# Kernel optimization log

Hardware: AMD Instinct MI355X
Metric: run time of the kernel (lower is better)

The kernel has to match this reference:

```python
import jax, jax.numpy as jnp
import numpy as np

B, S, T, H, NH, G, E, I, R, L = 256, 256, 16, 1024, 8, 3, 8, 4096, 256, 3
GTEMP, RTEMP, TOPK_G, NEG = 1.0, 1.0, 2, -1e9

_W = {
    'ts_in_w': (3*H, H), 'ts_out_w': (H, H),
    'st_in_w': (3*H, H), 'st_out_w': (H, H),
    'ca_in_w': (3*H, H), 'ca_out_w': (H, H),
    'opq_w': (H, H), 'fuse_w': (H, 3*H), 'gate_w': (H, 3*H),
    'bs_w': (R, H), 'bt_w': (R, H), 'bo_w': (H, R),
    'cond_w': (H, 2*H), 'gr_w': (G, H), 'er_w': (G, E, H),
    'e_w1': (G, E, I, H), 'e_w2': (G, E, H, I), 'cls_w': (L, H),
}
_B = {
    'ts_in_b': (3*H,), 'ts_out_b': (H,), 'st_in_b': (3*H,), 'st_out_b': (H,),
    'ca_in_b': (3*H,), 'ca_out_b': (H,), 'fuse_b': (H,), 'gate_b': (H,),
    'bs_b': (R,), 'bt_b': (R,), 'bo_b': (H,), 'cond_b': (H,),
    'gr_b': (G,), 'er_b': (G, E), 'e_b1': (G, E, I), 'e_b2': (G, E, H),
    'cls_b': (L,), 'ln_b': (3*H,),
}


def setup_inputs() -> dict:
    key = jax.random.key(0)
    out = {}
    out['h_sent'] = jax.random.normal(jax.random.fold_in(key, 1), (B, S, H), dtype=jnp.float32)
    out['h_term'] = jax.random.normal(jax.random.fold_in(key, 2), (B, T, H), dtype=jnp.float32)
    for i, (name, shp) in enumerate(_W.items()):
        out[name] = 0.02 * jax.random.normal(jax.random.fold_in(key, 100 + i), shp, dtype=jnp.float32)
    for name, shp in _B.items():
        out[name] = jnp.zeros(shp, dtype=jnp.float32)
    out['ln_g'] = jnp.ones((3*H,), dtype=jnp.float32)
    return out


def _mha(q, k, v, w_in, b_in, w_out, b_out):
    # torch nn.MultiheadAttention (batch_first, eval mode / no dropout)
    wq, wk, wv = jnp.split(w_in, 3, axis=0)
    bq, bk, bv = jnp.split(b_in, 3, axis=0)
    Q, K, V = q @ wq.T + bq, k @ wk.T + bk, v @ wv.T + bv
    b, lq, _ = Q.shape
    lk = K.shape[1]
    d = H // NH
    Q = Q.reshape(b, lq, NH, d).transpose(0, 2, 1, 3)
    K = K.reshape(b, lk, NH, d).transpose(0, 2, 1, 3)
    V = V.reshape(b, lk, NH, d).transpose(0, 2, 1, 3)
    att = jax.nn.softmax(jnp.einsum('bhqd,bhkd->bhqk', Q, K) * (1.0 / d ** 0.5), axis=-1)
    o = jnp.einsum('bhqk,bhkd->bhqd', att, V).transpose(0, 2, 1, 3).reshape(b, lq, H)
    return o @ w_out.T + b_out


def _ln(x, g, b, eps=1e-5):
    mu = x.mean(-1, keepdims=True)
    var = ((x - mu) ** 2).mean(-1, keepdims=True)
    return (x - mu) * jax.lax.rsqrt(var + eps) * g + b


def reference(h_sent, h_term, ts_in_w, ts_in_b, ts_out_w, ts_out_b,
              st_in_w, st_in_b, st_out_w, st_out_b,
              ca_in_w, ca_in_b, ca_out_w, ca_out_b,
              opq_w, ln_g, ln_b, fuse_w, fuse_b, gate_w, gate_b,
              bs_w, bs_b, bt_w, bt_b, bo_w, bo_b, cond_w, cond_b,
              gr_w, gr_b, er_w, er_b, e_w1, e_b1, e_w2, e_b2, cls_w, cls_b):
    # --- co-attention fusion ---
    t2s = _mha(h_term, h_sent, h_sent, ts_in_w, ts_in_b, ts_out_w, ts_out_b)  # [B,T,H]
    s2t = _mha(h_sent, h_term, h_term, st_in_w, st_in_b, st_out_w, st_out_b)  # [B,S,H]
    v_term = t2s.mean(axis=1)   # [B,H]
    v_sent = s2t.mean(axis=1)   # [B,H]
    oq = h_term @ opq_w.T       # opinion query projection (no bias)
    v_op = _mha(oq, h_sent, h_sent, ca_in_w, ca_in_b, ca_out_w, ca_out_b).mean(axis=1)
    cat3 = jnp.concatenate([v_sent, v_term, v_op], axis=-1)        # [B,3H]
    fused_lin = _ln(cat3, ln_g, ln_b) @ fuse_w.T + fuse_b           # [B,H]
    g = jax.nn.sigmoid(cat3 @ gate_w.T + gate_b)                    # [B,H]
    bil = ((v_sent @ bs_w.T + bs_b) * (v_term @ bt_w.T + bt_b)) @ bo_w.T + bo_b
    fused = g * fused_lin + (1.0 - g) * bil                         # [B,H]
    cond = jnp.concatenate([fused, v_term], axis=-1) @ cond_w.T + cond_b  # [B,H]
    # --- hierarchical group -> expert soft routing ---
    glog = fused @ gr_w.T + gr_b                                    # [B,G]
    thr = jax.lax.top_k(glog, TOPK_G)[0][:, -1:]
    glog = jnp.where(glog >= thr, glog, NEG)
    gp = jax.nn.softmax(glog / GTEMP, axis=-1)                      # [B,G]
    elog = jnp.einsum('bh,geh->bge', cond, er_w) + er_b             # [B,G,E]
    ep = jax.nn.softmax(elog / RTEMP, axis=-1)
    # all experts applied densely (soft routing); FFN experts: GELU MLP
    h1 = jax.nn.gelu(jnp.einsum('bh,geih->bgei', fused, e_w1) + e_b1, approximate=False)
    y = jnp.einsum('bgei,gehi->bgeh', h1, e_w2) + e_b2              # [B,G,E,H]
    moe = jnp.einsum('bge,bgeh->bh', gp[:, :, None] * ep, y)
    out = fused + moe                                               # residual merge
    return out @ cls_w.T + cls_b                                    # [B,L]
```

## Files before the change

### kernel.cpp

```cpp
#include <hip/hip_runtime.h>
#include <math.h>


#define B_    256
#define S_    256
#define T_    16
#define H_    1024
#define NH_   8
#define DH_   128
#define M128_ 128
#define G_    3
#define E_    8
#define I_    4096
#define R_    256
#define L_    3
#define GE_   24

using bf16x8 = __attribute__((ext_vector_type(8))) __bf16;
using f32x4  = __attribute__((ext_vector_type(4))) float;

__device__ inline float wave_sum(float v) {
    for (int o = 32; o > 0; o >>= 1) v += __shfl_xor(v, o);
    return v;
}
__device__ inline float wave_max(float v) {
    for (int o = 32; o > 0; o >>= 1) v = fmaxf(v, __shfl_xor(v, o));
    return v;
}

template <int ACT>
__global__ __launch_bounds__(256) void sgemm2_k(
    const float* __restrict__ Ap, const float* __restrict__ Bp,
    const float* __restrict__ biasp, const float* __restrict__ roffp,
    float* __restrict__ Cf,
    int K, int m2shift, int zshift,
    long sA1, long sA2, long sAz1, long sAz2,
    long ldb, long sBz1, long sBz2, long sBia1, long sBia2,
    long sC1, long sC2, long sCz1, long sCz2, long sR1, long sR2,
    float scale)
{
    const int z  = blockIdx.z;
    const int z1 = z >> zshift;
    const int z2 = z & ((1 << zshift) - 1);
    const int m2mask = (1 << m2shift) - 1;
    const int row0 = blockIdx.y * 128;
    const int col0 = blockIdx.x * 128;
    const float* Ab = Ap + (long)z1 * sAz1 + (long)z2 * sAz2;
    const float* Bb = Bp + (long)z1 * sBz1 + (long)z2 * sBz2;
    const float* biasb = biasp ? biasp + (long)z1 * sBia1 + (long)z2 * sBia2 : nullptr;
    const float* roffb = roffp ? roffp + (long)z1 * sR1 + (long)z2 * sR2 : nullptr;

    __shared__ __bf16 Ahs[128 * 40];
    __shared__ __bf16 Als[128 * 40];
    __shared__ __bf16 Bhs[128 * 40];
    __shared__ __bf16 Bls[128 * 40];

    const int tid  = threadIdx.x;
    const int lane = tid & 63;
    const int wid  = tid >> 6;
    const int wm = (wid >> 1) * 64;
    const int wn = (wid & 1) * 64;
    const int fr  = lane & 15;
    const int fkb = (lane >> 4) * 16;
    const int qrow = tid >> 2;
    const int c4   = tid & 3;

    f32x4 acc[4][4] = {};
    float4 pfa[2][2], pfb[2][2];

    auto loadAB = [&](int k0) {
#pragma unroll
        for (int rep = 0; rep < 2; ++rep) {
            const int row = qrow + rep * 64;
            const int r = row0 + row;
            const int r1 = r >> m2shift, r2 = r & m2mask;
            const float* srcA = Ab + (long)r1 * sA1 + (long)r2 * sA2 + k0 + c4 * 8;
            pfa[rep][0] = *(const float4*)srcA;
            pfa[rep][1] = *(const float4*)(srcA + 4);
            const float* srcB = Bb + (long)(col0 + row) * ldb + k0 + c4 * 8;
            pfb[rep][0] = *(const float4*)srcB;
            pfb[rep][1] = *(const float4*)(srcB + 4);
        }
    };

    loadAB(0);
    for (int k0 = 0; k0 < K; k0 += 32) {
        __syncthreads();
#pragma unroll
        for (int rep = 0; rep < 2; ++rep) {
            const int row = qrow + rep * 64;
            {
                const float fv[8] = {pfa[rep][0].x, pfa[rep][0].y, pfa[rep][0].z, pfa[rep][0].w,
                                     pfa[rep][1].x, pfa[rep][1].y, pfa[rep][1].z, pfa[rep][1].w};
                bf16x8 hi, lo;
#pragma unroll
                for (int j = 0; j < 8; ++j) {
                    const __bf16 h = (__bf16)fv[j];
                    hi[j] = h; lo[j] = (__bf16)(fv[j] - (float)h);
                }
                *(bf16x8*)&Ahs[row * 40 + c4 * 8] = hi;
                *(bf16x8*)&Als[row * 40 + c4 * 8] = lo;
            }
            {
                const float fv[8] = {pfb[rep][0].x, pfb[rep][0].y, pfb[rep][0].z, pfb[rep][0].w,
                                     pfb[rep][1].x, pfb[rep][1].y, pfb[rep][1].z, pfb[rep][1].w};
                bf16x8 hi, lo;
#pragma unroll
                for (int j = 0; j < 8; ++j) {
                    const __bf16 h = (__bf16)fv[j];
                    hi[j] = h; lo[j] = (__bf16)(fv[j] - (float)h);
                }
                *(bf16x8*)&Bhs[row * 40 + c4 * 8] = hi;
                *(bf16x8*)&Bls[row * 40 + c4 * 8] = lo;
            }
        }
        __syncthreads();
        if (k0 + 32 < K) loadAB(k0 + 32);

        bf16x8 bh4[4], bl4[4];
#pragma unroll
        for (int n = 0; n < 4; ++n) {
            bh4[n] = *(const bf16x8*)((const char*)&Bhs[(wn + n * 16 + fr) * 40] + fkb);
            bl4[n] = *(const bf16x8*)((const char*)&Bls[(wn + n * 16 + fr) * 40] + fkb);
        }
#pragma unroll
        for (int m = 0; m < 4; ++m) {
            const bf16x8 ah = *(const bf16x8*)((const char*)&Ahs[(wm + m * 16 + fr) * 40] + fkb);
            const bf16x8 al = *(const bf16x8*)((const char*)&Als[(wm + m * 16 + fr) * 40] + fkb);
#pragma unroll
            for (int n = 0; n < 4; ++n) {
                acc[m][n] = __builtin_amdgcn_mfma_f32_16x16x32_bf16(ah, bh4[n], acc[m][n], 0, 0, 0);
                acc[m][n] = __builtin_amdgcn_mfma_f32_16x16x32_bf16(ah, bl4[n], acc[m][n], 0, 0, 0);
                acc[m][n] = __builtin_amdgcn_mfma_f32_16x16x32_bf16(al, bh4[n], acc[m][n], 0, 0, 0);
            }
        }
    }

    float* Cfb = Cf + (long)z1 * sCz1 + (long)z2 * sCz2;
    const int lr4 = (lane >> 4) * 4;
#pragma unroll
    for (int m = 0; m < 4; ++m) {
#pragma unroll
        for (int r = 0; r < 4; ++r) {
            const int rr = row0 + wm + m * 16 + lr4 + r;
            const int r1 = rr >> m2shift, r2 = rr & m2mask;
            const float ro = roffb ? roffb[rr] : 0.f;
            const long cb = (long)r1 * sC1 + (long)r2 * sC2;
#pragma unroll
            for (int n = 0; n < 4; ++n) {
                const int cc = col0 + wn + n * 16 + fr;
                float v = (acc[m][n][r] + ro) * scale;
                if (biasp) v += biasb[cc];
                if (ACT == 2) v = 1.0f / (1.0f + expf(-v));
                Cfb[cb + cc] = v;
            }
        }
    }
}

static void sg2(hipStream_t s, int act,
                const float* A, const float* B, const float* bias, const float* roff,
                float* C, int gx, int gy, int gz,
                int K, int m2shift, int zshift,
                long sA1, long sA2, long sAz1, long sAz2,
                long ldb, long sBz1, long sBz2, long sBia1, long sBia2,
                long sC1, long sC2, long sCz1, long sCz2, long sR1, long sR2,
                float scale)
{
    dim3 g(gx, gy, gz), b(256);
#define S2ARGS A, B, bias, roff, C, K, m2shift, zshift, sA1, sA2, sAz1, sAz2, \
               ldb, sBz1, sBz2, sBia1, sBia2, sC1, sC2, sCz1, sCz2, sR1, sR2, scale
    if (act == 2) sgemm2_k<2><<<g, b, 0, s>>>(S2ARGS);
    else          sgemm2_k<0><<<g, b, 0, s>>>(S2ARGS);
#undef S2ARGS
}

template <int ABF16, int BSING, int ACT, int WMUL, int OUTH>
__global__ __launch_bounds__(512) void sgemm256_k(
    const void* __restrict__ Ap, const float* __restrict__ Bp,
    const float* __restrict__ biasp, const float* __restrict__ wmulp,
    float* __restrict__ Cf, __bf16* __restrict__ Ch,
    int K, long sA1, long sAz, long ldb, long sBz, long sBz2, int bzshift,
    long sBias, long sC1, long sCz, long sWr, float scale)
{
    const int z    = blockIdx.z;
    const int col0 = blockIdx.x * 128;
    const int z1 = z >> bzshift;
    const int z2 = z - (z1 << bzshift);
    const float* Bb = Bp + (long)z1 * sBz + (long)z2 * sBz2;
    const float* biasb = biasp ? biasp + (long)z1 * sBias : nullptr;

    __shared__ __bf16 Ah[256 * 40];
    __shared__ __bf16 Al[ABF16 ? 64 : 256 * 40];
    __shared__ __bf16 Bh[128 * 40];
    __shared__ __bf16 Bl[BSING ? 64 : 128 * 40];

    const int tid  = threadIdx.x;
    const int lane = tid & 63;
    const int wid  = tid >> 6;
    const int wm = (wid >> 1) * 64;
    const int wn = (wid & 1) * 64;
    const int fr  = lane & 15;
    const int fkb = (lane >> 4) * 16;

    f32x4 acc[4][4] = {};
    bf16x8 pfah[2];
    float4 pfaf[2][2];
    float4 pfb[2];

    auto loadAB = [&](int k0) {
#pragma unroll
        for (int rep = 0; rep < 2; ++rep) {
            const int idx = tid + rep * 512;
            const int row = idx >> 2;
            const int cc4 = idx & 3;
            if (ABF16) {
                pfah[rep] = *(const bf16x8*)((const __bf16*)Ap + (long)z * sAz +
                                             (long)row * sA1 + k0 + cc4 * 8);
            } else {
                const float* src = (const float*)Ap + (long)z * sAz +
                                   (long)row * sA1 + k0 + cc4 * 8;
                pfaf[rep][0] = *(const float4*)src;
                pfaf[rep][1] = *(const float4*)(src + 4);
            }
        }
        {
            const int row = tid >> 2;
            const int cc4 = tid & 3;
            const float* src = Bb + (long)(col0 + row) * ldb + k0 + cc4 * 8;
            pfb[0] = *(const float4*)src;
            pfb[1] = *(const float4*)(src + 4);
        }
    };

    loadAB(0);
    for (int k0 = 0; k0 < K; k0 += 32) {
        __syncthreads();
#pragma unroll
        for (int rep = 0; rep < 2; ++rep) {
            const int idx = tid + rep * 512;
            const int row = idx >> 2;
            const int cc4 = idx & 3;
            if (ABF16) {
                *(bf16x8*)&Ah[row * 40 + cc4 * 8] = pfah[rep];
            } else {
                const float fv[8] = {pfaf[rep][0].x, pfaf[rep][0].y, pfaf[rep][0].z, pfaf[rep][0].w,
                                     pfaf[rep][1].x, pfaf[rep][1].y, pfaf[rep][1].z, pfaf[rep][1].w};
                bf16x8 hi, lo;
#pragma unroll
                for (int j = 0; j < 8; ++j) {
                    const __bf16 h = (__bf16)fv[j];
                    hi[j] = h; lo[j] = (__bf16)(fv[j] - (float)h);
                }
                *(bf16x8*)&Ah[row * 40 + cc4 * 8] = hi;
                *(bf16x8*)&Al[row * 40 + cc4 * 8] = lo;
            }
        }
        {
            const int row = tid >> 2;
            const int cc4 = tid & 3;
            const float fv[8] = {pfb[0].x, pfb[0].y, pfb[0].z, pfb[0].w,
                                 pfb[1].x, pfb[1].y, pfb[1].z, pfb[1].w};
            bf16x8 hi, lo;
#pragma unroll
            for (int j = 0; j < 8; ++j) {
                const __bf16 h = (__bf16)fv[j];
                hi[j] = h;
                if (!BSING) lo[j] = (__bf16)(fv[j] - (float)h);
            }
            *(bf16x8*)&Bh[row * 40 + cc4 * 8] = hi;
            if (!BSING) *(bf16x8*)&Bl[row * 40 + cc4 * 8] = lo;
        }
        __syncthreads();
        if (k0 + 32 < K) loadAB(k0 + 32);

        bf16x8 bh4[4], bl4[4];
#pragma unroll
        for (int n = 0; n < 4; ++n) {
            bh4[n] = *(const bf16x8*)((const char*)&Bh[(wn + n * 16 + fr) * 40] + fkb);
            if (!BSING) bl4[n] = *(const bf16x8*)((const char*)&Bl[(wn + n * 16 + fr) * 40] + fkb);
        }
#pragma unroll
        for (int m = 0; m < 4; ++m) {
            const bf16x8 ah = *(const bf16x8*)((const char*)&Ah[(wm + m * 16 + fr) * 40] + fkb);
            bf16x8 al;
            if (!ABF16) al = *(const bf16x8*)((const char*)&Al[(wm + m * 16 + fr) * 40] + fkb);
#pragma unroll
            for (int n = 0; n < 4; ++n) {
                acc[m][n] = __builtin_amdgcn_mfma_f32_16x16x32_bf16(ah, bh4[n], acc[m][n], 0, 0, 0);
                if (!BSING) acc[m][n] = __builtin_amdgcn_mfma_f32_16x16x32_bf16(ah, bl4[n], acc[m][n], 0, 0, 0);
                if (!ABF16) acc[m][n] = __builtin_amdgcn_mfma_f32_16x16x32_bf16(al, bh4[n], acc[m][n], 0, 0, 0);
            }
        }
    }

    const int lr4 = (lane >> 4) * 4;
#pragma unroll
    for (int m = 0; m < 4; ++m) {
#pragma unroll
        for (int r = 0; r < 4; ++r) {
            const int rr = wm + m * 16 + lr4 + r;
#pragma unroll
            for (int n = 0; n < 4; ++n) {
                const int cc = col0 + wn + n * 16 + fr;
                float v = acc[m][n][r] * scale;
                if (biasp) v += biasb[cc];
                if (ACT == 1) v = 0.5f * v * (1.0f + erff(v * 0.70710678118654752f));
                if (WMUL) v *= wmulp[(long)rr * sWr + z];
                if (OUTH) Ch[(long)z * sCz + (long)rr * sC1 + cc] = (__bf16)v;
                else      Cf[(long)z * sCz + (long)rr * sC1 + cc] = v;
            }
        }
    }
}

#define BM 64
#define BN 64
#define BK 16
__global__ __launch_bounds__(256) void gemm_k(
    const float* __restrict__ Ap, const float* __restrict__ Bp,
    const float* __restrict__ biasp, float* __restrict__ Cp,
    int M, int N, int K, long sA1, long ldb, long sC1)
{
    const int row0 = blockIdx.y * BM;
    const int col0 = blockIdx.x * BN;
    const int tid = threadIdx.x;
    __shared__ float As[BK][BM + 4];
    __shared__ float Bs[BK][BN + 4];
    float acc[4][4] = {};
    const int tm = (tid >> 4) << 2;
    const int tn = (tid & 15) << 2;
    for (int k0 = 0; k0 < K; k0 += BK) {
        {
            const int i = tid << 2;
            const int m = i >> 4, kk = i & 15;
            const int r = row0 + m;
            float4 v = make_float4(0.f, 0.f, 0.f, 0.f);
            if (r < M) v = *(const float4*)(Ap + (long)r * sA1 + k0 + kk);
            As[kk + 0][m] = v.x; As[kk + 1][m] = v.y;
            As[kk + 2][m] = v.z; As[kk + 3][m] = v.w;
        }
        {
            const int i = tid << 2;
            const int n = i >> 4, kk = i & 15;
            const int c = col0 + n;
            float4 v = make_float4(0.f, 0.f, 0.f, 0.f);
            if (c < N) v = *(const float4*)(Bp + (long)c * ldb + k0 + kk);
            Bs[kk + 0][n] = v.x; Bs[kk + 1][n] = v.y;
            Bs[kk + 2][n] = v.z; Bs[kk + 3][n] = v.w;
        }
        __syncthreads();
#pragma unroll
        for (int kk = 0; kk < BK; ++kk) {
            const float4 av = *(const float4*)&As[kk][tm];
            const float4 bv = *(const float4*)&Bs[kk][tn];
            acc[0][0] += av.x * bv.x; acc[0][1] += av.x * bv.y;
            acc[0][2] += av.x * bv.z; acc[0][3] += av.x * bv.w;
            acc[1][0] += av.y * bv.x; acc[1][1] += av.y * bv.y;
            acc[1][2] += av.y * bv.z; acc[1][3] += av.y * bv.w;
            acc[2][0] += av.z * bv.x; acc[2][1] += av.z * bv.y;
            acc[2][2] += av.z * bv.z; acc[2][3] += av.z * bv.w;
            acc[3][0] += av.w * bv.x; acc[3][1] += av.w * bv.y;
            acc[3][2] += av.w * bv.z; acc[3][3] += av.w * bv.w;
        }
        __syncthreads();
    }
#pragma unroll
    for (int i2 = 0; i2 < 4; ++i2) {
        const int r = row0 + tm + i2;
        if (r >= M) continue;
        float* crow = Cp + (long)r * sC1;
#pragma unroll
        for (int j = 0; j < 4; ++j) {
            const int c = col0 + tn + j;
            if (c >= N) continue;
            float v = acc[i2][j];
            if (biasp) v += biasp[c];
            crow[c] = v;
        }
    }
}

static void g_launch(hipStream_t s, const float* A, const float* Bw, const float* bias,
                     float* C, int M, int N, int K, long sA1, long ldb, long sC1)
{
    dim3 grid((N + BN - 1) / BN, (M + BM - 1) / BM, 1);
    gemm_k<<<grid, dim3(256), 0, s>>>(A, Bw, bias, C, M, N, K, sA1, ldb, sC1);
}

template <int ACT>
__global__ void kred_k(const float* __restrict__ part, const float* __restrict__ bias,
                       float* __restrict__ out, int n, long stride, int nz, int biasMask)
{
    const int i = blockIdx.x * blockDim.x + threadIdx.x;
    if (i >= n) return;
    float v = 0.f;
    for (int z = 0; z < nz; ++z) v += part[(long)z * stride + i];
    if (bias) v += bias[i & biasMask];
    if (ACT == 2) v = 1.0f / (1.0f + expf(-v));
    out[i] = v;
}

__global__ void tT_k(const float* __restrict__ src, float* __restrict__ dst, int R, int C)
{
    __shared__ float t[32][33];
    const int c0 = blockIdx.x * 32, r0 = blockIdx.y * 32;
    const int tx = threadIdx.x & 31, ty = threadIdx.x >> 5;
#pragma unroll
    for (int i = 0; i < 4; ++i) {
        const int r = ty + i * 8;
        t[r][tx] = src[(long)(r0 + r) * C + c0 + tx];
    }
    __syncthreads();
#pragma unroll
    for (int i = 0; i < 4; ++i) {
        const int r = ty + i * 8;
        dst[(long)(c0 + r) * R + r0 + tx] = t[tx][r];
    }
}

__global__ void cpy_k(const float* __restrict__ src, float* __restrict__ dst, int n4)
{
    const int i = blockIdx.x * blockDim.x + threadIdx.x;
    if (i < n4) ((float4*)dst)[i] = ((const float4*)src)[i];
}

__global__ void biascat_k(const float* __restrict__ ts_b, const float* __restrict__ ca_b,
                          const float* __restrict__ st_b,
                          const float* __restrict__ ts_ob, const float* __restrict__ ca_ob,
                          const float* __restrict__ st_ob,
                          float* __restrict__ BCAT, float* __restrict__ BKCAT,
                          float* __restrict__ WVB, float* __restrict__ WOB)
{
    const int i = blockIdx.x * blockDim.x + threadIdx.x;
    if (i >= 1024) return;
    BCAT[i] = ts_b[i]; BCAT[1024 + i] = ca_b[i];
    BCAT[2048 + i] = st_b[1024 + i]; BCAT[3072 + i] = st_b[2048 + i];
    BKCAT[i] = ts_b[1024 + i]; BKCAT[1024 + i] = ca_b[1024 + i]; BKCAT[2048 + i] = st_b[i];
    WVB[i] = ts_b[2048 + i]; WVB[1024 + i] = ca_b[2048 + i];
    WOB[i] = ts_ob[i]; WOB[1024 + i] = ca_ob[i]; WOB[2048 + i] = st_ob[i];
}

__global__ void headdot3_k(const float* __restrict__ QALL, const float* __restrict__ BKCAT,
                           float* __restrict__ out)
{
    const int idx = blockIdx.x * blockDim.x + threadIdx.x;
    if (idx >= 3 * B_ * T_ * NH_) return;
    const int mod = idx >> 15;
    const int b = (idx >> 7) & 255;
    const int t = (idx >> 3) & 15;
    const int h = idx & 7;
    const float* q = QALL + (long)(b * 16 + t) * 4096 + mod * 1024 + h * 128;
    const float* bb = BKCAT + mod * 1024 + h * 128;
    float sum = 0.f;
    for (int k = 0; k < DH_; ++k) sum += q[k] * bb[k];
    out[idx] = sum;
}

__global__ __launch_bounds__(64) void softpb_k(const float* __restrict__ sc3,
                                               float* __restrict__ pbar,
                                               float* __restrict__ attm)
{
    const int blk = blockIdx.x;
    const int h = blk & 7;
    const int b = (blk >> 3) & 255;
    const int mod = blk >> 11;
    const int lane = threadIdx.x;
    const float* base = sc3 + (long)mod * 8388608 + (long)b * 32768 + (long)h * 256;
    float v[16][4];
#pragma unroll
    for (int t = 0; t < 16; ++t) {
        const float* rowp = base + (long)t * 2048;
#pragma unroll
        for (int j = 0; j < 4; ++j) v[t][j] = rowp[j * 64 + lane];
    }
    if (mod < 2) {
        float pb[4] = {0.f, 0.f, 0.f, 0.f};
#pragma unroll
        for (int t = 0; t < 16; ++t) {
            float m = fmaxf(fmaxf(v[t][0], v[t][1]), fmaxf(v[t][2], v[t][3]));
            m = wave_max(m);
            const float e0 = expf(v[t][0] - m), e1 = expf(v[t][1] - m);
            const float e2 = expf(v[t][2] - m), e3 = expf(v[t][3] - m);
            const float inv = 1.f / wave_sum(e0 + e1 + e2 + e3);
            pb[0] += e0 * inv; pb[1] += e1 * inv; pb[2] += e2 * inv; pb[3] += e3 * inv;
        }
        float* pd = pbar + (long)mod * 524288 + (long)b * 2048 + h * 256;
#pragma unroll
        for (int j = 0; j < 4; ++j) pd[j * 64 + lane] = pb[j] * (1.0f / 16.f);
    } else {
        float am[16];
#pragma unroll
        for (int t = 0; t < 16; ++t) am[t] = 0.f;
#pragma unroll
        for (int j = 0; j < 4; ++j) {
            float mx = v[0][j];
#pragma unroll
            for (int t = 1; t < 16; ++t) mx = fmaxf(mx, v[t][j]);
            float e[16];
            float sum = 0.f;
#pragma unroll
            for (int t = 0; t < 16; ++t) { e[t] = expf(v[t][j] - mx); sum += e[t]; }
            const float inv = 1.f / sum;
#pragma unroll
            for (int t = 0; t < 16; ++t) am[t] += e[t] * inv;
        }
#pragma unroll
        for (int t = 0; t < 16; ++t) {
            const float sm = wave_sum(am[t]) * (1.0f / 256.f);
            if (lane == 0) attm[b * 128 + t * 8 + h] = sm;
        }
    }
}

__global__ __launch_bounds__(256) void ctxw2_k(const float* __restrict__ pbar,
                                               const float* __restrict__ hs,
                                               float* __restrict__ part)
{
    const int b = blockIdx.x;
    const int sc = blockIdx.y;
    __shared__ float pl[16][64];
    const int tid = threadIdx.x;
    for (int i = tid; i < 16 * 64; i += 256) {
        const int row = i >> 6;
        const int mod = row >> 3;
        pl[row][i & 63] = pbar[(long)mod * 524288 + (long)b * 2048 +
                               (row & 7) * 256 + sc * 64 + (i & 63)];
    }
    __syncthreads();
    const int k0 = tid * 4;
    float4 acc[16] = {};
    const float* hb = hs + (long)b * S_ * H_ + (long)sc * 64 * H_;
    for (int s = 0; s < 64; ++s) {
        const float4 vv = *(const float4*)(hb + (long)s * H_ + k0);
#pragma unroll
        for (int j = 0; j < 16; ++j) {
            const float p = pl[j][s];
            acc[j].x += p * vv.x; acc[j].y += p * vv.y;
            acc[j].z += p * vv.z; acc[j].w += p * vv.w;
        }
    }
    float* ob = part + (long)sc * 4194304;
#pragma unroll
    for (int j = 0; j < 16; ++j) {
        const int mod = j >> 3, hh = j & 7;
        *(float4*)(ob + (long)mod * 2097152 + (long)b * 8192 + hh * 1024 + k0) = acc[j];
    }
}

__global__ void ohead2_k(const float* __restrict__ attm, const float* __restrict__ QALL,
                         float* __restrict__ outb)
{
    const int idx = blockIdx.x * blockDim.x + threadIdx.x;
    if (idx >= B_ * H_) return;
    const int c = idx & (H_ - 1);
    const int b = idx >> 10;
    float sv = 0.f;
#pragma unroll
    for (int t = 0; t < T_; ++t)
        sv += attm[b * M128_ + t * NH_ + (c >> 7)] * QALL[(long)(b * 16 + t) * 4096 + 3072 + c];
    outb[idx] = sv;
}

__global__ void cat3_k(const float* __restrict__ vs, const float* __restrict__ vt,
                       const float* __restrict__ vo, float* __restrict__ out)
{
    const int idx = blockIdx.x * blockDim.x + threadIdx.x;
    if (idx >= B_ * 3 * H_) return;
    const int k = idx % (3 * H_);
    const int b = idx / (3 * H_);
    float v;
    if (k < H_)          v = vs[b * H_ + k];
    else if (k < 2 * H_) v = vt[b * H_ + k - H_];
    else                 v = vo[b * H_ + k - 2 * H_];
    out[idx] = v;
}

__global__ void ln_k(const float* __restrict__ cat3, const float* __restrict__ g,
                     const float* __restrict__ bta, float* __restrict__ out)
{
    const int b = blockIdx.x;
    const int tid = threadIdx.x;
    __shared__ float buf[3 * H_];
    __shared__ float red[4];
    const float* src = cat3 + (long)b * 3 * H_;
    float sv = 0.f;
    for (int i = tid; i < 3 * H_; i += 256) { const float x = src[i]; buf[i] = x; sv += x; }
    sv = wave_sum(sv);
    if ((tid & 63) == 0) red[tid >> 6] = sv;
    __syncthreads();
    const float mu = (red[0] + red[1] + red[2] + red[3]) * (1.f / (3 * H_));
    __syncthreads();
    float s2 = 0.f;
    for (int i = tid; i < 3 * H_; i += 256) { const float d0 = buf[i] - mu; s2 += d0 * d0; }
    s2 = wave_sum(s2);
    if ((tid & 63) == 0) red[tid >> 6] = s2;
    __syncthreads();
    const float var = (red[0] + red[1] + red[2] + red[3]) * (1.f / (3 * H_));
    const float rstd = rsqrtf(var + 1e-5f);
    float* dst = out + (long)b * 3 * H_;
    for (int i = tid; i < 3 * H_; i += 256)
        dst[i] = (buf[i] - mu) * rstd * g[i] + bta[i];
}

__global__ void mulf_k(const float* __restrict__ a, const float* __restrict__ b2,
                       float* __restrict__ out, int n)
{
    const int idx = blockIdx.x * blockDim.x + threadIdx.x;
    if (idx < n) out[idx] = a[idx] * b2[idx];
}

__global__ void fuse_k(const float* __restrict__ g, const float* __restrict__ flin,
                       const float* __restrict__ bil, float* __restrict__ fused,
                       __bf16* __restrict__ fusedh)
{
    const int idx = blockIdx.x * blockDim.x + threadIdx.x;
    if (idx >= B_ * H_) return;
    const float gg = g[idx];
    const float v = gg * flin[idx] + (1.f - gg) * bil[idx];
    fused[idx] = v;
    fusedh[idx] = (__bf16)v;
}

__global__ void catfv_k(const float* __restrict__ fused, const float* __restrict__ vt,
                        float* __restrict__ out)
{
    const int idx = blockIdx.x * blockDim.x + threadIdx.x;
    if (idx >= B_ * 2 * H_) return;
    const int k = idx % (2 * H_);
    const int b = idx / (2 * H_);
    out[idx] = (k < H_) ? fused[b * H_ + k] : vt[b * H_ + k - H_];
}

__global__ void route_k(const float* __restrict__ glog, float* __restrict__ gp)
{
    const int b = blockIdx.x * blockDim.x + threadIdx.x;
    if (b >= B_) return;
    const float x0 = glog[b * 3], x1 = glog[b * 3 + 1], x2 = glog[b * 3 + 2];
    const float m1 = fmaxf(x0, fmaxf(x1, x2));
    float thr;
    if (x0 == m1)      thr = fmaxf(x1, x2);
    else if (x1 == m1) thr = fmaxf(x0, x2);
    else               thr = fmaxf(x0, x1);
    const float y0 = (x0 >= thr) ? x0 : -1e9f;
    const float y1 = (x1 >= thr) ? x1 : -1e9f;
    const float y2 = (x2 >= thr) ? x2 : -1e9f;
    const float mm = fmaxf(y0, fmaxf(y1, y2));
    const float e0 = expf(y0 - mm), e1 = expf(y1 - mm), e2 = expf(y2 - mm);
    const float inv = 1.f / (e0 + e1 + e2);
    gp[b * 3] = e0 * inv; gp[b * 3 + 1] = e1 * inv; gp[b * 3 + 2] = e2 * inv;
}

__global__ void epsm_k(float* __restrict__ elog, const float* __restrict__ gp)
{
    const int idx = blockIdx.x * blockDim.x + threadIdx.x;
    if (idx >= B_ * G_) return;
    float* p = elog + (long)idx * E_;
    float m = p[0];
#pragma unroll
    for (int e = 1; e < E_; ++e) m = fmaxf(m, p[e]);
    float sum = 0.f;
    float v[E_];
#pragma unroll
    for (int e = 0; e < E_; ++e) { v[e] = expf(p[e] - m); sum += v[e]; }
    const float w = gp[idx] / sum;
#pragma unroll
    for (int e = 0; e < E_; ++e) p[e] = v[e] * w;
}

__global__ void moefinal_k(const float* __restrict__ part, const float* __restrict__ fused,
                           const float* __restrict__ wsc, const float* __restrict__ e_b2,
                           float* __restrict__ res)
{
    const int idx = blockIdx.x * blockDim.x + threadIdx.x;
    if (idx >= B_ * H_) return;
    const int b = idx >> 10;
    const int h = idx & (H_ - 1);
    float acc = fused[idx];
#pragma unroll 8
    for (int z = 0; z < 48; ++z) acc += part[(long)z * (B_ * H_) + idx];
    float ba = 0.f;
#pragma unroll
    for (int ge = 0; ge < GE_; ++ge) ba += wsc[b * GE_ + ge] * e_b2[ge * H_ + h];
    res[idx] = acc + ba;
}

extern "C" void kernel_launch(void* const* d_in, const int* in_sizes, int n_in,
                              void* d_out, int out_size, void* d_ws, size_t ws_size,
                              hipStream_t stream)
{
    const float* h_sent  = (const float*)d_in[0];
    const float* h_term  = (const float*)d_in[1];
    const float* ts_in_w = (const float*)d_in[2];
    const float* ts_out_w= (const float*)d_in[3];
    const float* st_in_w = (const float*)d_in[4];
    const float* st_out_w= (const float*)d_in[5];
    const float* ca_in_w = (const float*)d_in[6];
    const float* ca_out_w= (const float*)d_in[7];
    const float* opq_w   = (const float*)d_in[8];
    const float* fuse_w  = (const float*)d_in[9];
    const float* gate_w  = (const float*)d_in[10];
    const float* bs_w    = (const float*)d_in[11];
    const float* bt_w    = (const float*)d_in[12];
    const float* bo_w    = (const float*)d_in[13];
    const float* cond_w  = (const float*)d_in[14];
    const float* gr_w    = (const float*)d_in[15];
    const float* er_w    = (const float*)d_in[16];
    const float* e_w1    = (const float*)d_in[17];
    const float* e_w2    = (const float*)d_in[18];
    const float* cls_w   = (const float*)d_in[19];
    const float* ts_in_b = (const float*)d_in[20];
    const float* ts_out_b= (const float*)d_in[21];
    const float* st_in_b = (const float*)d_in[22];
    const float* st_out_b= (const float*)d_in[23];
    const float* ca_in_b = (const float*)d_in[24];
    const float* ca_out_b= (const float*)d_in[25];
    const float* fuse_b  = (const float*)d_in[26];
    const float* gate_b  = (const float*)d_in[27];
    const float* bs_b    = (const float*)d_in[28];
    const float* bt_b    = (const float*)d_in[29];
    const float* bo_b    = (const float*)d_in[30];
    const float* cond_b  = (const float*)d_in[31];
    const float* gr_b    = (const float*)d_in[32];
    const float* er_b    = (const float*)d_in[33];
    const float* e_b1    = (const float*)d_in[34];
    const float* e_b2    = (const float*)d_in[35];
    const float* cls_b   = (const float*)d_in[36];
    const float* ln_b    = (const float*)d_in[37];
    const float* ln_g    = (const float*)d_in[38];
    (void)in_sizes; (void)n_in; (void)out_size; (void)ws_size;

    float* ws = (float*)d_ws;
    size_t off = 0;
    auto allocF = [&](size_t n) { float* p = ws + off; off += (n + 63) & ~(size_t)63; return p; };

    float* QALL  = allocF(16777216);
    float* WCAT  = allocF(4194304);
    float* BCAT  = allocF(4096);
    float* BKCAT = allocF(3072);
    float* wT3   = allocF(3145728);
    float* opqT  = allocF(1048576);
    float* WVCAT = allocF(2097152);
    float* WVB   = allocF(2048);
    float* WOCAT = allocF(3145728);
    float* WOB   = allocF(3072);
    float* OFFS3 = allocF(98304);
    float* BIG3  = allocF(100663296);
    float* SC3   = allocF(25165824);
    float* PBAR3 = allocF(1048576);
    float* CTXB3 = allocF(4194304);
    float* PARTC = allocF(16777216);
    float* OBAR3 = allocF(786432);
    float* VOUT3 = allocF(786432);
    float* ATTM  = allocF(32768);
    float* CAT3  = allocF(786432);
    float* LNC   = allocF(786432);
    float* FLIN  = allocF(262144);
    float* GATE  = allocF(262144);
    float* BSV   = allocF(65536);
    float* BTV   = allocF(65536);
    float* PROD  = allocF(65536);
    float* BIL   = allocF(262144);
    float* FUSED = allocF(262144);
    float* FUSEDH= allocF(131072);
    float* CATFV = allocF(524288);
    float* COND  = allocF(262144);
    float* GLOG  = allocF(1024);
    float* GP    = allocF(1024);
    float* ELOG  = allocF(8192);
    float* RES   = allocF(262144);
    float* PARTF = allocF(1048576);
    float* H1Wf  = allocF(12582912);
    float* PART  = allocF(12582912);
    __bf16* FUSEDbf = (__bf16*)FUSEDH;
    __bf16* H1W     = (__bf16*)H1Wf;
    float* VTERM = VOUT3;
    float* VOP   = VOUT3 + 262144;
    float* VSENT = VOUT3 + 524288;

    hipStream_t s = stream;
    const float rscale = 0.08838834764831845f;

    cpy_k<<<dim3(1024), dim3(256), 0, s>>>(ts_in_w, WCAT, 262144);
    cpy_k<<<dim3(1024), dim3(256), 0, s>>>(st_in_w + 1048576, WCAT + 2097152, 262144);
    cpy_k<<<dim3(1024), dim3(256), 0, s>>>(st_in_w + 2097152, WCAT + 3145728, 262144);
    cpy_k<<<dim3(1024), dim3(256), 0, s>>>(ts_in_w + 2097152, WVCAT, 262144);
    cpy_k<<<dim3(1024), dim3(256), 0, s>>>(ca_in_w + 2097152, WVCAT + 1048576, 262144);
    cpy_k<<<dim3(1024), dim3(256), 0, s>>>(ts_out_w, WOCAT, 262144);
    cpy_k<<<dim3(1024), dim3(256), 0, s>>>(ca_out_w, WOCAT + 1048576, 262144);
    cpy_k<<<dim3(1024), dim3(256), 0, s>>>(st_out_w, WOCAT + 2097152, 262144);
    biascat_k<<<dim3(4), dim3(256), 0, s>>>(ts_in_b, ca_in_b, st_in_b,
                                            ts_out_b, ca_out_b, st_out_b,
                                            BCAT, BKCAT, WVB, WOB);
    tT_k<<<dim3(32, 32), dim3(256), 0, s>>>(ts_in_w + 1048576, wT3, 1024, 1024);
    tT_k<<<dim3(32, 32), dim3(256), 0, s>>>(ca_in_w + 1048576, wT3 + 1048576, 1024, 1024);
    tT_k<<<dim3(32, 32), dim3(256), 0, s>>>(st_in_w, wT3 + 2097152, 1024, 1024);
    tT_k<<<dim3(32, 32), dim3(256), 0, s>>>(opq_w, opqT, 1024, 1024);

    sg2(s, 0, ca_in_w, opqT, nullptr, nullptr, WCAT + 1048576,
        8, 8, 1, 1024, 12, 0, 0, 1024, 0, 0, 1024, 0, 0, 0, 0,
        0, 1024, 0, 0, 0, 0, 1.f);

    sg2(s, 0, h_term, WCAT, BCAT, nullptr, QALL,
        32, 32, 1, 1024, 12, 0, 0, 1024, 0, 0, 1024, 0, 0, 0, 0,
        0, 4096, 0, 0, 0, 0, 1.f);

    headdot3_k<<<dim3(384), dim3(256), 0, s>>>(QALL, BKCAT, OFFS3);

    sg2(s, 0, QALL, wT3, nullptr, nullptr, BIG3,
        8, 32, 24, 128, 4, 3,
        65536, 4096, 1024, 128,
        1024, 1048576, 128, 0, 0,
        131072, 8192, 33554432, 1024, 0, 0, 1.f);

    sg2(s, 0, BIG3, h_sent, nullptr, OFFS3, SC3,
        2, 1, 768, 1024, 12, 8,
        0, 1024, 33554432, 131072,
        1024, 0, 262144, 0, 0,
        0, 256, 8388608, 32768, 32768, 128, rscale);

    softpb_k<<<dim3(3 * B_ * NH_), dim3(64), 0, s>>>(SC3, PBAR3, ATTM);

    ctxw2_k<<<dim3(B_, 4), dim3(256), 0, s>>>(PBAR3, h_sent, PARTC);
    kred_k<0><<<dim3(4194304 / 256), dim3(256), 0, s>>>(PARTC, nullptr, CTXB3,
                                                        4194304, 4194304, 4, 0);
    sg2(s, 0, CTXB3, WVCAT, WVB, nullptr, OBAR3,
        1, 2, 16, 1024, 12, 3,
        0, 8192, 2097152, 1024,
        1024, 1048576, 131072, 1024, 128,
        0, 1024, 262144, 128, 0, 0, 1.f);

    ohead2_k<<<dim3((B_ * H_ + 255) / 256), dim3(256), 0, s>>>(ATTM, QALL, OBAR3 + 524288);

    sg2(s, 0, OBAR3, WOCAT, WOB, nullptr, VOUT3,
        8, 2, 3, 1024, 12, 0,
        0, 1024, 262144, 0,
        1024, 1048576, 0, 1024, 0,
        0, 1024, 262144, 0, 0, 0, 1.f);

    cat3_k<<<dim3((B_ * 3 * H_ + 255) / 256), dim3(256), 0, s>>>(VSENT, VTERM, VOP, CAT3);
    ln_k<<<dim3(B_), dim3(256), 0, s>>>(CAT3, ln_g, ln_b, LNC);
    sg2(s, 0, LNC, fuse_w, nullptr, nullptr, PARTF,
        8, 2, 4, 768, 12, 2, 0, 3072, 0, 768, 3072, 0, 768, 0, 0,
        0, 1024, 0, 262144, 0, 0, 1.f);
    kred_k<0><<<dim3(1024), dim3(256), 0, s>>>(PARTF, fuse_b, FLIN, 262144, 262144, 4, 1023);
    sg2(s, 0, CAT3, gate_w, nullptr, nullptr, PARTF,
        8, 2, 4, 768, 12, 2, 0, 3072, 0, 768, 3072, 0, 768, 0, 0,
        0, 1024, 0, 262144, 0, 0, 1.f);
    kred_k<2><<<dim3(1024), dim3(256), 0, s>>>(PARTF, gate_b, GATE, 262144, 262144, 4, 1023);
    sg2(s, 0, VSENT, bs_w, nullptr, nullptr, PARTF,
        2, 2, 4, 256, 12, 2, 0, 1024, 0, 256, 1024, 0, 256, 0, 0,
        0, 256, 0, 65536, 0, 0, 1.f);
    kred_k<0><<<dim3(256), dim3(256), 0, s>>>(PARTF, bs_b, BSV, 65536, 65536, 4, 255);
    sg2(s, 0, VTERM, bt_w, nullptr, nullptr, PARTF,
        2, 2, 4, 256, 12, 2, 0, 1024, 0, 256, 1024, 0, 256, 0, 0,
        0, 256, 0, 65536, 0, 0, 1.f);
    kred_k<0><<<dim3(256), dim3(256), 0, s>>>(PARTF, bt_b, BTV, 65536, 65536, 4, 255);
    mulf_k<<<dim3((B_ * R_ + 255) / 256), dim3(256), 0, s>>>(BSV, BTV, PROD, B_ * R_);
    sg2(s, 0, PROD, bo_w, nullptr, nullptr, PARTF,
        8, 2, 2, 128, 12, 1, 0, 256, 0, 128, 256, 0, 128, 0, 0,
        0, 1024, 0, 262144, 0, 0, 1.f);
    kred_k<0><<<dim3(1024), dim3(256), 0, s>>>(PARTF, bo_b, BIL, 262144, 262144, 2, 1023);
    fuse_k<<<dim3((B_ * H_ + 255) / 256), dim3(256), 0, s>>>(GATE, FLIN, BIL, FUSED, FUSEDbf);
    catfv_k<<<dim3((B_ * 2 * H_ + 255) / 256), dim3(256), 0, s>>>(FUSED, VTERM, CATFV);
    sg2(s, 0, CATFV, cond_w, nullptr, nullptr, PARTF,
        8, 2, 4, 512, 12, 2, 0, 2048, 0, 512, 2048, 0, 512, 0, 0,
        0, 1024, 0, 262144, 0, 0, 1.f);
    kred_k<0><<<dim3(1024), dim3(256), 0, s>>>(PARTF, cond_b, COND, 262144, 262144, 4, 1023);

    g_launch(s, FUSED, gr_w, gr_b, GLOG, B_, G_, H_, H_, H_, G_);
    route_k<<<dim3(1), dim3(256), 0, s>>>(GLOG, GP);
    g_launch(s, COND, er_w, er_b, ELOG, B_, GE_, H_, H_, H_, GE_);
    epsm_k<<<dim3(3), dim3(256), 0, s>>>(ELOG, GP);

    sgemm256_k<1, 1, 1, 1, 1><<<dim3(I_ / 128, 1, GE_), dim3(512), 0, s>>>(
        FUSEDbf, e_w1, e_b1, ELOG, nullptr, H1W,
        1024, H_, 0, H_, (long)I_ * H_, 0, 0, I_,
        (long)GE_ * I_, I_, GE_, 1.f);
    sgemm256_k<1, 1, 0, 0, 0><<<dim3(H_ / 128, 1, 2 * GE_), dim3(512), 0, s>>>(
        H1W, e_w2, nullptr, nullptr, PART, nullptr,
        2048, (long)GE_ * I_, 2048, I_, (long)H_ * I_, 2048, 1, 0,
        H_, (long)B_ * H_, 0, 1.f);
    moefinal_k<<<dim3(B_ * H_ / 256), dim3(256), 0, s>>>(PART, FUSED, ELOG, e_b2, RES);

    g_launch(s, RES, cls_w, cls_b, (float*)d_out, B_, L_, H_, H_, H_, L_);
}
```

Baseline: 1.636 ms.

## Batch weight prep copies into fused launches and retile score GEMM

Merges eight weight-copy launches into one multi-segment copy kernel and four transposes into one batched transpose kernel, cutting launch count. The large score GEMM is regridded so each block loops over two column chunks and z is reordered (batch-major with a z2 bound guard), so one block covers a 256-wide output span and nearby blocks share the same A rows. This trades fewer, larger blocks for less launch overhead and possibly better cache locality. The cost is less parallelism per launch and some idle blocks from the padded z dimension.

```diff
diff --git a/kernel.cpp b/kernel.cpp
--- a/kernel.cpp
+++ b/kernel.cpp
@@ -28,12 +28,12 @@
     return v;
 }
 
-template <int ACT>
+template <int ACT, int NCH>
 __global__ __launch_bounds__(256) void sgemm2_k(
     const float* __restrict__ Ap, const float* __restrict__ Bp,
     const float* __restrict__ biasp, const float* __restrict__ roffp,
     float* __restrict__ Cf,
-    int K, int m2shift, int zshift,
+    int K, int m2shift, int zshift, int z2max,
     long sA1, long sA2, long sAz1, long sAz2,
     long ldb, long sBz1, long sBz2, long sBia1, long sBia2,
     long sC1, long sC2, long sCz1, long sCz2, long sR1, long sR2,
@@ -42,9 +42,9 @@
     const int z  = blockIdx.z;
     const int z1 = z >> zshift;
     const int z2 = z & ((1 << zshift) - 1);
+    if (z2 >= z2max) return;
     const int m2mask = (1 << m2shift) - 1;
     const int row0 = blockIdx.y * 128;
-    const int col0 = blockIdx.x * 128;
     const float* Ab = Ap + (long)z1 * sAz1 + (long)z2 * sAz2;
     const float* Bb = Bp + (long)z1 * sBz1 + (long)z2 * sBz2;
     const float* biasb = biasp ? biasp + (long)z1 * sBia1 + (long)z2 * sBia2 : nullptr;
@@ -65,10 +65,9 @@
     const int qrow = tid >> 2;
     const int c4   = tid & 3;
 
-    f32x4 acc[4][4] = {};
     float4 pfa[2][2], pfb[2][2];
 
-    auto loadAB = [&](int k0) {
+    auto loadAB = [&](int k0, int col0) {
 #pragma unroll
         for (int rep = 0; rep < 2; ++rep) {
             const int row = qrow + rep * 64;
@@ -83,82 +82,86 @@
         }
     };
 
-    loadAB(0);
-    for (int k0 = 0; k0 < K; k0 += 32) {
-        __syncthreads();
-#pragma unroll
-        for (int rep = 0; rep < 2; ++rep) {
-            const int row = qrow + rep * 64;
-            {
-                const float fv[8] = {pfa[rep][0].x, pfa[rep][0].y, pfa[rep][0].z, pfa[rep][0].w,
-                                     pfa[rep][1].x, pfa[rep][1].y, pfa[rep][1].z, pfa[rep][1].w};
-                bf16x8 hi, lo;
-#pragma unroll
-                for (int j = 0; j < 8; ++j) {
-                    const __bf16 h = (__bf16)fv[j];
-                    hi[j] = h; lo[j] = (__bf16)(fv[j] - (float)h);
+    for (int ch = 0; ch < NCH; ++ch) {
+        const int col0 = (blockIdx.x * NCH + ch) * 128;
+        f32x4 acc[4][4] = {};
+        loadAB(0, col0);
+        for (int k0 = 0; k0 < K; k0 += 32) {
+            __syncthreads();
+#pragma unroll
+            for (int rep = 0; rep < 2; ++rep) {
+                const int row = qrow + rep * 64;
+                {
+                    const float fv[8] = {pfa[rep][0].x, pfa[rep][0].y, pfa[rep][0].z, pfa[rep][0].w,
+                                         pfa[rep][1].x, pfa[rep][1].y, pfa[rep][1].z, pfa[rep][1].w};
+                    bf16x8 hi, lo;
+#pragma unroll
+                    for (int j = 0; j < 8; ++j) {
+                        const __bf16 h = (__bf16)fv[j];
+                        hi[j] = h; lo[j] = (__bf16)(fv[j] - (float)h);
+                    }
+                    *(bf16x8*)&Ahs[row * 40 + c4 * 8] = hi;
+                    *(bf16x8*)&Als[row * 40 + c4 * 8] = lo;
                 }
-                *(bf16x8*)&Ahs[row * 40 + c4 * 8] = hi;
-                *(bf16x8*)&Als[row * 40 + c4 * 8] = lo;
+                {
+                    const float fv[8] = {pfb[rep][0].x, pfb[rep][0].y, pfb[rep][0].z, pfb[rep][0].w,
+                                         pfb[rep][1].x, pfb[rep][1].y, pfb[rep][1].z, pfb[rep][1].w};
+                    bf16x8 hi, lo;
+#pragma unroll
+                    for (int j = 0; j < 8; ++j) {
+                        const __bf16 h = (__bf16)fv[j];
+                        hi[j] = h; lo[j] = (__bf16)(fv[j] - (float)h);
+                    }
+                    *(bf16x8*)&Bhs[row * 40 + c4 * 8] = hi;
+                    *(bf16x8*)&Bls[row * 40 + c4 * 8] = lo;
+                }
             }
-            {
-                const float fv[8] = {pfb[rep][0].x, pfb[rep][0].y, pfb[rep][0].z, pfb[rep][0].w,
-                                     pfb[rep][1].x, pfb[rep][1].y, pfb[rep][1].z, pfb[rep][1].w};
-                bf16x8 hi, lo;
-#pragma unroll
-                for (int j = 0; j < 8; ++j) {
-                    const __bf16 h = (__bf16)fv[j];
-                    hi[j] = h; lo[j] = (__bf16)(fv[j] - (float)h);
+            __syncthreads();
+            if (k0 + 32 < K) loadAB(k0 + 32, col0);
+
+            bf16x8 bh4[4], bl4[4];
+#pragma unroll
+            for (int n = 0; n < 4; ++n) {
+                bh4[n] = *(const bf16x8*)((const char*)&Bhs[(wn + n * 16 + fr) * 40] + fkb);
+                bl4[n] = *(const bf16x8*)((const char*)&Bls[(wn + n * 16 + fr) * 40] + fkb);
+            }
+#pragma unroll
+            for (int m = 0; m < 4; ++m) {
+                const bf16x8 ah = *(const bf16x8*)((const char*)&Ahs[(wm + m * 16 + fr) * 40] + fkb);
+                const bf16x8 al = *(const bf16x8*)((const char*)&Als[(wm + m * 16 + fr) * 40] + fkb);
+#pragma unroll
+                for (int n = 0; n < 4; ++n) {
+                    acc[m][n] = __builtin_amdgcn_mfma_f32_16x16x32_bf16(ah, bh4[n], acc[m][n], 0, 0, 0);
+                    acc[m][n] = __builtin_amdgcn_mfma_f32_16x16x32_bf16(ah, bl4[n], acc[m][n], 0, 0, 0);
+                    acc[m][n] = __builtin_amdgcn_mfma_f32_16x16x32_bf16(al, bh4[n], acc[m][n], 0, 0, 0);
                 }
-                *(bf16x8*)&Bhs[row * 40 + c4 * 8] = hi;
-                *(bf16x8*)&Bls[row * 40 + c4 * 8] = lo;
             }
         }
-        __syncthreads();
-        if (k0 + 32 < K) loadAB(k0 + 32);
-
-        bf16x8 bh4[4], bl4[4];
-#pragma unroll
-        for (int n = 0; n < 4; ++n) {
-            bh4[n] = *(const bf16x8*)((const char*)&Bhs[(wn + n * 16 + fr) * 40] + fkb);
-            bl4[n] = *(const bf16x8*)((const char*)&Bls[(wn + n * 16 + fr) * 40] + fkb);
-        }
+
+        float* Cfb = Cf + (long)z1 * sCz1 + (long)z2 * sCz2;
+        const int lr4 = (lane >> 4) * 4;
 #pragma unroll
         for (int m = 0; m < 4; ++m) {
-            const bf16x8 ah = *(const bf16x8*)((const char*)&Ahs[(wm + m * 16 + fr) * 40] + fkb);
-            const bf16x8 al = *(const bf16x8*)((const char*)&Als[(wm + m * 16 + fr) * 40] + fkb);
-#pragma unroll
-            for (int n = 0; n < 4; ++n) {
-                acc[m][n] = __builtin_amdgcn_mfma_f32_16x16x32_bf16(ah, bh4[n], acc[m][n], 0, 0, 0);
-                acc[m][n] = __builtin_amdgcn_mfma_f32_16x16x32_bf16(ah, bl4[n], acc[m][n], 0, 0, 0);
-                acc[m][n] = __builtin_amdgcn_mfma_f32_16x16x32_bf16(al, bh4[n], acc[m][n], 0, 0, 0);
+#pragma unroll
+            for (int r = 0; r < 4; ++r) {
+                const int rr = row0 + wm + m * 16 + lr4 + r;
+                const int r1 = rr >> m2shift, r2 = rr & m2mask;
+                const float ro = roffb ? roffb[rr] : 0.f;
+                const long cb = (long)r1 * sC1 + (long)r2 * sC2;
+#pragma unroll
+                for (int n = 0; n < 4; ++n) {
+                    const int cc = col0 + wn + n * 16 + fr;
+                    float v = (acc[m][n][r] + ro) * scale;
+                    if (biasp) v += biasb[cc];
+                    if (ACT == 2) v = 1.0f / (1.0f + expf(-v));
+                    Cfb[cb + cc] = v;
+                }
             }
         }
     }
-
-    float* Cfb = Cf + (long)z1 * sCz1 + (long)z2 * sCz2;
-    const int lr4 = (lane >> 4) * 4;
-#pragma unroll
-    for (int m = 0; m < 4; ++m) {
-#pragma unroll
-        for (int r = 0; r < 4; ++r) {
-            const int rr = row0 + wm + m * 16 + lr4 + r;
-            const int r1 = rr >> m2shift, r2 = rr & m2mask;
-            const float ro = roffb ? roffb[rr] : 0.f;
-            const long cb = (long)r1 * sC1 + (long)r2 * sC2;
-#pragma unroll
-            for (int n = 0; n < 4; ++n) {
-                const int cc = col0 + wn + n * 16 + fr;
-                float v = (acc[m][n][r] + ro) * scale;
-                if (biasp) v += biasb[cc];
-                if (ACT == 2) v = 1.0f / (1.0f + expf(-v));
-                Cfb[cb + cc] = v;
-            }
-        }
-    }
-}
-
-static void sg2(hipStream_t s, int act,
+}
+
+static void sg2(hipStream_t s, int act, int nch, int z2max,
                 const float* A, const float* B, const float* bias, const float* roff,
                 float* C, int gx, int gy, int gz,
                 int K, int m2shift, int zshift,
@@ -168,10 +171,11 @@
                 float scale)
 {
     dim3 g(gx, gy, gz), b(256);
-#define S2ARGS A, B, bias, roff, C, K, m2shift, zshift, sA1, sA2, sAz1, sAz2, \
+#define S2ARGS A, B, bias, roff, C, K, m2shift, zshift, z2max, sA1, sA2, sAz1, sAz2, \
                ldb, sBz1, sBz2, sBia1, sBia2, sC1, sC2, sCz1, sCz2, sR1, sR2, scale
-    if (act == 2) sgemm2_k<2><<<g, b, 0, s>>>(S2ARGS);
-    else          sgemm2_k<0><<<g, b, 0, s>>>(S2ARGS);
+    if (nch == 2)      sgemm2_k<0, 2><<<g, b, 0, s>>>(S2ARGS);
+    else if (act == 2) sgemm2_k<2, 1><<<g, b, 0, s>>>(S2ARGS);
+    else               sgemm2_k<0, 1><<<g, b, 0, s>>>(S2ARGS);
 #undef S2ARGS
 }
 
@@ -401,28 +405,38 @@
     out[i] = v;
 }
 
-__global__ void tT_k(const float* __restrict__ src, float* __restrict__ dst, int R, int C)
+__global__ void cpy8_k(const float* s0, const float* s1, const float* s2, const float* s3,
+                       const float* s4, const float* s5, const float* s6, const float* s7,
+                       float* d0, float* d1, float* d2, float* d3,
+                       float* d4, float* d5, float* d6, float* d7)
+{
+    const int seg = blockIdx.x >> 10;
+    const int i = ((blockIdx.x & 1023) * 256 + threadIdx.x);
+    const float* srcs[8] = {s0, s1, s2, s3, s4, s5, s6, s7};
+    float* dsts[8] = {d0, d1, d2, d3, d4, d5, d6, d7};
+    ((float4*)dsts[seg])[i] = ((const float4*)srcs[seg])[i];
+}
+
+__global__ void tT4_k(const float* s0, const float* s1, const float* s2, const float* s3,
+                      float* d0, float* d1, float* d2, float* d3)
 {
     __shared__ float t[32][33];
-    const int c0 = blockIdx.x * 32, r0 = blockIdx.y * 32;
+    const int seg = blockIdx.y >> 5;
+    const float* src = seg == 0 ? s0 : seg == 1 ? s1 : seg == 2 ? s2 : s3;
+    float* dst = seg == 0 ? d0 : seg == 1 ? d1 : seg == 2 ? d2 : d3;
+    const int c0 = blockIdx.x * 32, r0 = (blockIdx.y & 31) * 32;
     const int tx = threadIdx.x & 31, ty = threadIdx.x >> 5;
 #pragma unroll
     for (int i = 0; i < 4; ++i) {
         const int r = ty + i * 8;
-        t[r][tx] = src[(long)(r0 + r) * C + c0 + tx];
+        t[r][tx] = src[(long)(r0 + r) * 1024 + c0 + tx];
     }
     __syncthreads();
 #pragma unroll
     for (int i = 0; i < 4; ++i) {
         const int r = ty + i * 8;
-        dst[(long)(c0 + r) * R + r0 + tx] = t[tx][r];
-    }
-}
-
-__global__ void cpy_k(const float* __restrict__ src, float* __restrict__ dst, int n4)
-{
-    const int i = blockIdx.x * blockDim.x + threadIdx.x;
-    if (i < n4) ((float4*)dst)[i] = ((const float4*)src)[i];
+        dst[(long)(c0 + r) * 1024 + r0 + tx] = t[tx][r];
+    }
 }
 
 __global__ void biascat_k(const float* __restrict__ ts_b, const float* __restrict__ ca_b,
@@ -780,51 +794,48 @@
 
     hipStream_t s = stream;
     const float rscale = 0.08838834764831845f;
-
-    cpy_k<<<dim3(1024), dim3(256), 0, s>>>(ts_in_w, WCAT, 262144);
-    cpy_k<<<dim3(1024), dim3(256), 0, s>>>(st_in_w + 1048576, WCAT + 2097152, 262144);
-    cpy_k<<<dim3(1024), dim3(256), 0, s>>>(st_in_w + 2097152, WCAT + 3145728, 262144);
-    cpy_k<<<dim3(1024), dim3(256), 0, s>>>(ts_in_w + 2097152, WVCAT, 262144);
-    cpy_k<<<dim3(1024), dim3(256), 0, s>>>(ca_in_w + 2097152, WVCAT + 1048576, 262144);
-    cpy_k<<<dim3(1024), dim3(256), 0, s>>>(ts_out_w, WOCAT, 262144);
-    cpy_k<<<dim3(1024), dim3(256), 0, s>>>(ca_out_w, WOCAT + 1048576, 262144);
-    cpy_k<<<dim3(1024), dim3(256), 0, s>>>(st_out_w, WOCAT + 2097152, 262144);
+    const int ZBIG = 1 << 30;
+
+    cpy8_k<<<dim3(8 * 1024), dim3(256), 0, s>>>(
+        ts_in_w, st_in_w + 1048576, st_in_w + 2097152, ts_in_w + 2097152,
+        ca_in_w + 2097152, ts_out_w, ca_out_w, st_out_w,
+        WCAT, WCAT + 2097152, WCAT + 3145728, WVCAT,
+        WVCAT + 1048576, WOCAT, WOCAT + 1048576, WOCAT + 2097152);
     biascat_k<<<dim3(4), dim3(256), 0, s>>>(ts_in_b, ca_in_b, st_in_b,
                                             ts_out_b, ca_out_b, st_out_b,
                                             BCAT, BKCAT, WVB, WOB);
-    tT_k<<<dim3(32, 32), dim3(256), 0, s>>>(ts_in_w + 1048576, wT3, 1024, 1024);
-    tT_k<<<dim3(32, 32), dim3(256), 0, s>>>(ca_in_w + 1048576, wT3 + 1048576, 1024, 1024);
-    tT_k<<<dim3(32, 32), dim3(256), 0, s>>>(st_in_w, wT3 + 2097152, 1024, 1024);
-    tT_k<<<dim3(32, 32), dim3(256), 0, s>>>(opq_w, opqT, 1024, 1024);
-
-    sg2(s, 0, ca_in_w, opqT, nullptr, nullptr, WCAT + 1048576,
+    tT4_k<<<dim3(32, 128), dim3(256), 0, s>>>(
+        ts_in_w + 1048576, ca_in_w + 1048576, st_in_w, opq_w,
+        wT3, wT3 + 1048576, wT3 + 2097152, opqT);
+
+    sg2(s, 0, 1, ZBIG, ca_in_w, opqT, nullptr, nullptr, WCAT + 1048576,
         8, 8, 1, 1024, 12, 0, 0, 1024, 0, 0, 1024, 0, 0, 0, 0,
         0, 1024, 0, 0, 0, 0, 1.f);
 
-    sg2(s, 0, h_term, WCAT, BCAT, nullptr, QALL,
+    sg2(s, 0, 1, ZBIG, h_term, WCAT, BCAT, nullptr, QALL,
         32, 32, 1, 1024, 12, 0, 0, 1024, 0, 0, 1024, 0, 0, 0, 0,
         0, 4096, 0, 0, 0, 0, 1.f);
 
     headdot3_k<<<dim3(384), dim3(256), 0, s>>>(QALL, BKCAT, OFFS3);
 
-    sg2(s, 0, QALL, wT3, nullptr, nullptr, BIG3,
+    sg2(s, 0, 1, ZBIG, QALL, wT3, nullptr, nullptr, BIG3,
         8, 32, 24, 128, 4, 3,
         65536, 4096, 1024, 128,
         1024, 1048576, 128, 0, 0,
         131072, 8192, 33554432, 1024, 0, 0, 1.f);
 
-    sg2(s, 0, BIG3, h_sent, nullptr, OFFS3, SC3,
-        2, 1, 768, 1024, 12, 8,
-        0, 1024, 33554432, 131072,
-        1024, 0, 262144, 0, 0,
-        0, 256, 8388608, 32768, 32768, 128, rscale);
+    sg2(s, 0, 2, 3, BIG3, h_sent, nullptr, OFFS3, SC3,
+        1, 1, 1024, 1024, 12, 2,
+        0, 1024, 131072, 33554432,
+        1024, 262144, 0, 0, 0,
+        0, 256, 32768, 8388608, 128, 32768, rscale);
 
     softpb_k<<<dim3(3 * B_ * NH_), dim3(64), 0, s>>>(SC3, PBAR3, ATTM);
 
     ctxw2_k<<<dim3(B_, 4), dim3(256), 0, s>>>(PBAR3, h_sent, PARTC);
     kred_k<0><<<dim3(4194304 / 256), dim3(256), 0, s>>>(PARTC, nullptr, CTXB3,
                                                         4194304, 4194304, 4, 0);
-    sg2(s, 0, CTXB3, WVCAT, WVB, nullptr, OBAR3,
+    sg2(s, 0, 1, ZBIG, CTXB3, WVCAT, WVB, nullptr, OBAR3,
         1, 2, 16, 1024, 12, 3,
         0, 8192, 2097152, 1024,
         1024, 1048576, 131072, 1024, 128,
@@ -832,7 +843,7 @@
 
     ohead2_k<<<dim3((B_ * H_ + 255) / 256), dim3(256), 0, s>>>(ATTM, QALL, OBAR3 + 524288);
 
-    sg2(s, 0, OBAR3, WOCAT, WOB, nullptr, VOUT3,
+    sg2(s, 0, 1, ZBIG, OBAR3, WOCAT, WOB, nullptr, VOUT3,
         8, 2, 3, 1024, 12, 0,
         0, 1024, 262144, 0,
         1024, 1048576, 0, 1024, 0,
@@ -840,30 +851,30 @@
 
     cat3_k<<<dim3((B_ * 3 * H_ + 255) / 256), dim3(256), 0, s>>>(VSENT, VTERM, VOP, CAT3);
     ln_k<<<dim3(B_), dim3(256), 0, s>>>(CAT3, ln_g, ln_b, LNC);
-    sg2(s, 0, LNC, fuse_w, nullptr, nullptr, PARTF,
+    sg2(s, 0, 1, ZBIG, LNC, fuse_w, nullptr, nullptr, PARTF,
         8, 2, 4, 768, 12, 2, 0, 3072, 0, 768, 3072, 0, 768, 0, 0,
         0, 1024, 0, 262144, 0, 0, 1.f);
     kred_k<0><<<dim3(1024), dim3(256), 0, s>>>(PARTF, fuse_b, FLIN, 262144, 262144, 4, 1023);
-    sg2(s, 0, CAT3, gate_w, nullptr, nullptr, PARTF,
+    sg2(s, 0, 1, ZBIG, CAT3, gate_w, nullptr, nullptr, PARTF,
         8, 2, 4, 768, 12, 2, 0, 3072, 0, 768, 3072, 0, 768, 0, 0,
         0, 1024, 0, 262144, 0, 0, 1.f);
     kred_k<2><<<dim3(1024), dim3(256), 0, s>>>(PARTF, gate_b, GATE, 262144, 262144, 4, 1023);
-    sg2(s, 0, VSENT, bs_w, nullptr, nullptr, PARTF,
+    sg2(s, 0, 1, ZBIG, VSENT, bs_w, nullptr, nullptr, PARTF,
         2, 2, 4, 256, 12, 2, 0, 1024, 0, 256, 1024, 0, 256, 0, 0,
         0, 256, 0, 65536, 0, 0, 1.f);
     kred_k<0><<<dim3(256), dim3(256), 0, s>>>(PARTF, bs_b, BSV, 65536, 65536, 4, 255);
-    sg2(s, 0, VTERM, bt_w, nullptr, nullptr, PARTF,
+    sg2(s, 0, 1, ZBIG, VTERM, bt_w, nullptr, nullptr, PARTF,
         2, 2, 4, 256, 12, 2, 0, 1024, 0, 256, 1024, 0, 256, 0, 0,
         0, 256, 0, 65536, 0, 0, 1.f);
     kred_k<0><<<dim3(256), dim3(256), 0, s>>>(PARTF, bt_b, BTV, 65536, 65536, 4, 255);
     mulf_k<<<dim3((B_ * R_ + 255) / 256), dim3(256), 0, s>>>(BSV, BTV, PROD, B_ * R_);
-    sg2(s, 0, PROD, bo_w, nullptr, nullptr, PARTF,
+    sg2(s, 0, 1, ZBIG, PROD, bo_w, nullptr, nullptr, PARTF,
         8, 2, 2, 128, 12, 1, 0, 256, 0, 128, 256, 0, 128, 0, 0,
         0, 1024, 0, 262144, 0, 0, 1.f);
     kred_k<0><<<dim3(1024), dim3(256), 0, s>>>(PARTF, bo_b, BIL, 262144, 262144, 2, 1023);
     fuse_k<<<dim3((B_ * H_ + 255) / 256), dim3(256), 0, s>>>(GATE, FLIN, BIL, FUSED, FUSEDbf);
     catfv_k<<<dim3((B_ * 2 * H_ + 255) / 256), dim3(256), 0, s>>>(FUSED, VTERM, CATFV);
-    sg2(s, 0, CATFV, cond_w, nullptr, nullptr, PARTF,
+    sg2(s, 0, 1, ZBIG, CATFV, cond_w, nullptr, nullptr, PARTF,
         8, 2, 4, 512, 12, 2, 0, 2048, 0, 512, 2048, 0, 512, 0, 0,
         0, 1024, 0, 262144, 0, 0, 1.f);
     kred_k<0><<<dim3(1024), dim3(256), 0, s>>>(PARTF, cond_b, COND, 262144, 262144, 4, 1023);
```

After: 1.627 ms. No clear change (-0.5%).
